# Kernel tuning notes

Hardware: AMD Instinct MI355X
Metric: run time of the kernel (lower is better)

The kernel has to match this reference:

```python
import jax, jax.numpy as jnp
import numpy as np
import math

NB_STEPS = 50  # matches init kwarg nb_steps


def cc_quadrature(nb_steps):
    # Clenshaw-Curtis weights/nodes, identical to UMNN's compute_cc_weights.
    lam = np.arange(nb_steps + 1, dtype=np.float64).reshape(-1, 1)
    lam = np.cos((lam @ lam.T) * math.pi / nb_steps)
    lam[:, 0] = 0.5
    lam[:, -1] = 0.5 * lam[:, -1]
    lam = lam * 2.0 / nb_steps
    W = np.arange(nb_steps + 1, dtype=np.float64).reshape(-1, 1)
    W[np.arange(1, nb_steps + 1, 2)] = 0
    W = 2.0 / (1.0 - W ** 2)
    W[0] = 1
    W[np.arange(1, nb_steps + 1, 2)] = 0
    cc_weights = (lam.T @ W).astype(np.float32)                 # [K, 1]
    steps = np.cos(np.arange(nb_steps + 1, dtype=np.float64).reshape(-1, 1)
                   * math.pi / nb_steps).astype(np.float32)     # [K, 1]
    return jnp.asarray(cc_weights), jnp.asarray(steps)


def integrand_mlp(xh, W1, b1, W2, b2, W3, b3, W4, b4):
    y = jax.nn.relu(jnp.einsum('bkd,hd->bkh', xh, W1) + b1)
    y = jax.nn.relu(jnp.einsum('bkh,gh->bkg', y, W2) + b2)
    y = jax.nn.relu(jnp.einsum('bkg,fg->bkf', y, W3) + b3)
    y = jnp.einsum('bkf,of->bko', y, W4) + b4
    return jax.nn.elu(y) + 1.0


def setup_inputs() -> dict:
    key = jax.random.key(0)
    ks = jax.random.split(key, 10)
    B, HD, IN_D = 16384, 128, 64
    x = jax.random.normal(ks[0], (B, 1), dtype=jnp.float32)
    h = jax.random.normal(ks[1], (B, IN_D - 1), dtype=jnp.float32)
    def lin(k, fan_out, fan_in):
        return jax.random.normal(k, (fan_out, fan_in), dtype=jnp.float32) / np.sqrt(fan_in)
    return {
        'x': x, 'h': h,
        'W1': lin(ks[2], HD, IN_D), 'b1': jax.random.normal(ks[3], (HD,), dtype=jnp.float32) * 0.01,
        'W2': lin(ks[4], HD, HD),   'b2': jax.random.normal(ks[5], (HD,), dtype=jnp.float32) * 0.01,
        'W3': lin(ks[6], HD, HD),   'b3': jax.random.normal(ks[7], (HD,), dtype=jnp.float32) * 0.01,
        'W4': lin(ks[8], 1, HD),    'b4': jax.random.normal(ks[9], (1,), dtype=jnp.float32) * 0.01,
    }


def reference(x, h, W1, b1, W2, b2, W3, b3, W4, b4):
    cc_w, steps = cc_quadrature(NB_STEPS)          # [K,1], [K,1]
    xmax = jnp.max(x) + 10.0
    x0 = x                                          # [B,1]
    xT = jnp.zeros_like(x) + xmax                   # xfinal broadcast
    # quadrature points X_steps: [B, K, 1]
    X = x0[:, None, :] + (xT - x0)[:, None, :] * (steps[None, :, :] + 1.0) * 0.5
    B, K = X.shape[0], X.shape[1]
    hK = jnp.broadcast_to(h[:, None, :], (B, K, h.shape[1]))
    xh = jnp.concatenate([X, hK], axis=-1)          # [B, K, in_d]
    f = integrand_mlp(xh, W1, b1, W2, b2, W3, b3, W4, b4)  # [B, K, 1]
    z = jnp.sum(f * cc_w[None, :, :], axis=1)       # [B, 1]
    return z * (xT - x0) * 0.5
```

## Files before the change

### kernel.cpp

```cpp
#include <hip/hip_runtime.h>
#include <hip/hip_bf16.h>
#include <math.h>


#define B_N    16384
#define KQ     51
#define HD     128
#define IND    64
#define BLK    128
#define RPB    16
#define GRID   (B_N / RPB)
#define TPB    (RPB * KQ / 16)

typedef __attribute__((ext_vector_type(8))) short short8;
typedef __attribute__((ext_vector_type(4))) float f32x4;

union S8U { short8 s8; unsigned u[4]; };

__device__ __forceinline__ unsigned short f2bf(float f) {
    __hip_bfloat16 t = __float2bfloat16(f);
    return *reinterpret_cast<unsigned short*>(&t);
}

#if defined(__gfx950__) && defined(__has_builtin)
#if __has_builtin(__builtin_amdgcn_cvt_pk_bf16_f32)
#define HAVE_PK_BF16 1
#endif
#endif

__device__ __forceinline__ unsigned pk_bf16(float lo, float hi) {
#ifdef HAVE_PK_BF16
    typedef __attribute__((ext_vector_type(2))) __bf16 bfv2;
    bfv2 r = __builtin_amdgcn_cvt_pk_bf16_f32(lo, hi);
    return *reinterpret_cast<unsigned*>(&r);
#else
    return (unsigned)f2bf(lo) | ((unsigned)f2bf(hi) << 16);
#endif
}

__device__ __forceinline__ float bf_lo(unsigned u) {
    return __uint_as_float(u << 16);
}
__device__ __forceinline__ float bf_hi(unsigned u) {
    return __uint_as_float(u & 0xffff0000u);
}

__launch_bounds__(BLK, 2)
__global__ void umnn_fused(const float* __restrict__ x,  const float* __restrict__ h,
                           const float* __restrict__ W1, const float* __restrict__ b1,
                           const float* __restrict__ W2, const float* __restrict__ b2,
                           const float* __restrict__ W3, const float* __restrict__ b3,
                           const float* __restrict__ W4, const float* __restrict__ b4,
                           float* __restrict__ out)
{
    __shared__ __align__(16) float hpL[RPB * HD];
    __shared__ __align__(16) char  y2x[2][4096];
    __shared__ __align__(16) float hshT[63 * 20];
    __shared__ float vs[RPB * KQ + 16];
    __shared__ float xL[RPB];
    __shared__ float sSteps[KQ], sCcw[KQ];
    __shared__ float red2[2];

    const int tid  = threadIdx.x;
    const int w    = tid >> 6;
    const int lane = tid & 63;
    const int q    = lane >> 4;
    const int lm   = lane & 15;
    const int swz  = lm & 7;
    const int rowBase = blockIdx.x * RPB;

    if (tid < KQ) {
        const int j = tid;
        const float pi50 = 0.06283185307179586f;
        sSteps[j] = __cosf((float)j * pi50);
        float s = 0.0f;
        for (int i = 0; i <= 50; i += 2) {
            float Wi = (i == 0) ? 1.0f : 2.0f / (1.0f - (float)(i * i));
            float lam;
            if (j == 0) lam = 0.5f;
            else {
                int mp = (i * j) % 100;
                lam = __cosf((float)mp * pi50);
                if (j == 50) lam *= 0.5f;
            }
            s += (lam * 0.04f) * Wi;
        }
        sCcw[j] = s;
    }
    {
        const f32x4* x4 = (const f32x4*)x;
        float mx = -1e30f;
        for (int i = tid; i < B_N / 4; i += BLK) {
            f32x4 v = x4[i];
            mx = fmaxf(fmaxf(mx, fmaxf(v[0], v[1])), fmaxf(v[2], v[3]));
        }
        #pragma unroll
        for (int d = 32; d > 0; d >>= 1) mx = fmaxf(mx, __shfl_xor(mx, d));
        if (lane == 0) red2[w] = mx;
    }
    for (int i = tid; i < RPB * 63; i += BLK) {
        int r = i / 63, d = i - r * 63;
        hshT[d * 20 + r] = h[rowBase * 63 + i];
    }
    if (tid < RPB) xL[tid] = x[rowBase + tid];
    __syncthreads();

    const float xmax = fmaxf(red2[0], red2[1]) + 10.0f;

    {
        const int n = tid;
        float acc[RPB];
        const float b1v = b1[n];
        #pragma unroll
        for (int r = 0; r < RPB; ++r) acc[r] = b1v;
        const float* wr = W1 + n * IND + 1;
        #pragma unroll 1
        for (int d = 0; d < IND - 1; ++d) {
            float wv = wr[d];
            const float* ht = hshT + d * 20;
            #pragma unroll
            for (int rc = 0; rc < RPB / 4; ++rc) {
                f32x4 hv = *(const f32x4*)(ht + rc * 4);
                acc[rc * 4 + 0] = fmaf(wv, hv[0], acc[rc * 4 + 0]);
                acc[rc * 4 + 1] = fmaf(wv, hv[1], acc[rc * 4 + 1]);
                acc[rc * 4 + 2] = fmaf(wv, hv[2], acc[rc * 4 + 2]);
                acc[rc * 4 + 3] = fmaf(wv, hv[3], acc[rc * 4 + 3]);
            }
        }
        #pragma unroll
        for (int r = 0; r < RPB; ++r) hpL[r * HD + n] = acc[r];
    }
    __syncthreads();

    if (w == 0) {
        float w1x[32];
        #pragma unroll
        for (int kk = 0; kk < 4; ++kk)
            #pragma unroll
            for (int j = 0; j < 8; ++j)
                w1x[kk * 8 + j] = W1[(kk * 32 + q * 8 + j) * IND];

        short8  W2A[8][4];
        unsigned b2p[16];
        #pragma unroll
        for (int nt = 0; nt < 8; ++nt) {
            #pragma unroll
            for (int kk = 0; kk < 4; ++kk) {
                const float* p2 = W2 + (nt * 16 + lm) * HD + kk * 32 + q * 8;
                S8U a2;
                #pragma unroll
                for (int j = 0; j < 4; ++j)
                    a2.u[j] = pk_bf16(p2[2 * j], p2[2 * j + 1]);
                W2A[nt][kk] = a2.s8;
            }
            b2p[2 * nt + 0] = pk_bf16(b2[nt * 16 + q * 4 + 0], b2[nt * 16 + q * 4 + 1]);
            b2p[2 * nt + 1] = pk_bf16(b2[nt * 16 + q * 4 + 2], b2[nt * 16 + q * 4 + 3]);
        }

        #pragma unroll 1
        for (int tt = 0; tt < TPB; ++tt) {
            const int s    = tt * 16 + lm;
            const unsigned row = (unsigned)s / KQ;
            const int k    = s - (int)row * KQ;
            const float x0 = xL[row];
            const float X  = fmaf((xmax - x0) * 0.5f, sSteps[k] + 1.0f, x0);
            short8 Y1[4];
            #pragma unroll
            for (int kk = 0; kk < 4; ++kk) {
                const float* hp = hpL + row * HD + kk * 32 + q * 8;
                f32x4 ha = *(const f32x4*)hp;
                f32x4 hb = *(const f32x4*)(hp + 4);
                S8U u;
                u.u[0] = pk_bf16(fmaxf(fmaf(X, w1x[kk*8+0], ha[0]), 0.f),
                                 fmaxf(fmaf(X, w1x[kk*8+1], ha[1]), 0.f));
                u.u[1] = pk_bf16(fmaxf(fmaf(X, w1x[kk*8+2], ha[2]), 0.f),
                                 fmaxf(fmaf(X, w1x[kk*8+3], ha[3]), 0.f));
                u.u[2] = pk_bf16(fmaxf(fmaf(X, w1x[kk*8+4], hb[0]), 0.f),
                                 fmaxf(fmaf(X, w1x[kk*8+5], hb[1]), 0.f));
                u.u[3] = pk_bf16(fmaxf(fmaf(X, w1x[kk*8+6], hb[2]), 0.f),
                                 fmaxf(fmaf(X, w1x[kk*8+7], hb[3]), 0.f));
                Y1[kk] = u.s8;
            }

            f32x4 C[8];
            #pragma unroll
            for (int nt = 0; nt < 8; ++nt) {
                unsigned u0 = b2p[2 * nt], u1 = b2p[2 * nt + 1];
                C[nt][0] = bf_lo(u0); C[nt][1] = bf_hi(u0);
                C[nt][2] = bf_lo(u1); C[nt][3] = bf_hi(u1);
            }
            #pragma unroll
            for (int kk = 0; kk < 4; ++kk)
                #pragma unroll
                for (int nt = 0; nt < 8; ++nt)
                    C[nt] = __builtin_amdgcn_mfma_f32_16x16x32_bf16(W2A[nt][kk], Y1[kk], C[nt], 0, 0, 0);

            char* myY2 = y2x[tt & 1];
            #pragma unroll
            for (int nt = 0; nt < 8; ++nt) {
                unsigned lo = pk_bf16(fmaxf(C[nt][0], 0.f), fmaxf(C[nt][1], 0.f));
                unsigned hi = pk_bf16(fmaxf(C[nt][2], 0.f), fmaxf(C[nt][3], 0.f));
                *(int2*)(myY2 + lm * 256 + (((2*nt + (q>>1)) ^ swz) << 4) + ((q & 1) << 3))
                    = make_int2((int)lo, (int)hi);
            }
            __syncthreads();
        }
    } else {
        short8  W3A[8][4];
        unsigned b3p[16];
        f32x4   W4c[8];
        #pragma unroll
        for (int nt = 0; nt < 8; ++nt) {
            #pragma unroll
            for (int kk = 0; kk < 4; ++kk) {
                const float* p3 = W3 + (nt * 16 + lm) * HD + kk * 32 + q * 8;
                S8U a3;
                #pragma unroll
                for (int j = 0; j < 4; ++j)
                    a3.u[j] = pk_bf16(p3[2 * j], p3[2 * j + 1]);
                W3A[nt][kk] = a3.s8;
            }
            b3p[2 * nt + 0] = pk_bf16(b3[nt * 16 + q * 4 + 0], b3[nt * 16 + q * 4 + 1]);
            b3p[2 * nt + 1] = pk_bf16(b3[nt * 16 + q * 4 + 2], b3[nt * 16 + q * 4 + 3]);
            W4c[nt] = *(const f32x4*)(W4 + nt * 16 + q * 4);
        }
        const float b4v = b4[0];

        #pragma unroll 1
        for (int tt = 0; tt < TPB; ++tt) {
            __syncthreads();
            const char* myY2 = y2x[tt & 1];
            short8 Y2[4];
            #pragma unroll
            for (int kk = 0; kk < 4; ++kk)
                Y2[kk] = *(const short8*)(myY2 + lm * 256 + (((kk*4 + q) ^ swz) << 4));

            f32x4 C[8];
            #pragma unroll
            for (int nt = 0; nt < 8; ++nt) {
                unsigned u0 = b3p[2 * nt], u1 = b3p[2 * nt + 1];
                C[nt][0] = bf_lo(u0); C[nt][1] = bf_hi(u0);
                C[nt][2] = bf_lo(u1); C[nt][3] = bf_hi(u1);
            }
            #pragma unroll
            for (int kk = 0; kk < 4; ++kk)
                #pragma unroll
                for (int nt = 0; nt < 8; ++nt)
                    C[nt] = __builtin_amdgcn_mfma_f32_16x16x32_bf16(W3A[nt][kk], Y2[kk], C[nt], 0, 0, 0);

            float p = 0.f;
            #pragma unroll
            for (int nt = 0; nt < 8; ++nt) {
                p = fmaf(fmaxf(C[nt][0], 0.f), W4c[nt][0], p);
                p = fmaf(fmaxf(C[nt][1], 0.f), W4c[nt][1], p);
                p = fmaf(fmaxf(C[nt][2], 0.f), W4c[nt][2], p);
                p = fmaf(fmaxf(C[nt][3], 0.f), W4c[nt][3], p);
            }
            p += __shfl_xor(p, 16);
            p += __shfl_xor(p, 32);
            if (lane < 16) vs[tt * 16 + lm] = p;
        }

        {
            const int r   = lane >> 2;
            const int sub = lane & 3;
            float a = 0.f;
            #pragma unroll 1
            for (int j = 0; j < 13; ++j) {
                int k = sub + 4 * j;
                if (k < KQ) {
                    float y4 = vs[r * KQ + k] + b4v;
                    float f  = (y4 > 0.f) ? (y4 + 1.f) : __expf(y4);
                    a = fmaf(f, sCcw[k], a);
                }
            }
            a += __shfl_xor(a, 1);
            a += __shfl_xor(a, 2);
            if (sub == 0)
                out[rowBase + r] = a * (xmax - xL[r]) * 0.5f;
        }
    }
}

extern "C" void kernel_launch(void* const* d_in, const int* in_sizes, int n_in,
                              void* d_out, int out_size, void* d_ws, size_t ws_size,
                              hipStream_t stream)
{
    const float* x  = (const float*)d_in[0];
    const float* h  = (const float*)d_in[1];
    const float* W1 = (const float*)d_in[2];
    const float* b1 = (const float*)d_in[3];
    const float* W2 = (const float*)d_in[4];
    const float* b2 = (const float*)d_in[5];
    const float* W3 = (const float*)d_in[6];
    const float* b3 = (const float*)d_in[7];
    const float* W4 = (const float*)d_in[8];
    const float* b4 = (const float*)d_in[9];
    float* out = (float*)d_out;

    umnn_fused<<<GRID, BLK, 0, stream>>>(x, h, W1, b1, W2, b2, W3, b3,
                                         W4, b4, out);
}
```

Before: 172.7 us.

## Split layer-2/3 MFMA work across four waves with a triple-buffered Y1 pipeline

Doubles the block to four waves. Two waves compute layer 2 and two compute layer 3, each wave owning half of the output tiles. Layer-1 activations are now built cooperatively into a three-slot shared-memory ring one tile ahead, and the layer-3 partial dot products land in two buffers that are summed in the final quadrature step. This is meant to remove the serial producer/consumer imbalance and the halved MFMA throughput per wave, at the cost of more barriers, more shared memory, and fewer registers per thread under launch_bounds(256,3).

```diff
diff --git a/kernel.cpp b/kernel.cpp
--- a/kernel.cpp
+++ b/kernel.cpp
@@ -7,10 +7,10 @@
 #define KQ     51
 #define HD     128
 #define IND    64
-#define BLK    128
+#define BLK    256
 #define RPB    16
 #define GRID   (B_N / RPB)
-#define TPB    (RPB * KQ / 16)
+#define TPB    ((RPB * KQ) / 16)
 
 typedef __attribute__((ext_vector_type(8))) short short8;
 typedef __attribute__((ext_vector_type(4))) float f32x4;
@@ -45,7 +45,7 @@
     return __uint_as_float(u & 0xffff0000u);
 }
 
-__launch_bounds__(BLK, 2)
+__launch_bounds__(BLK, 3)
 __global__ void umnn_fused(const float* __restrict__ x,  const float* __restrict__ h,
                            const float* __restrict__ W1, const float* __restrict__ b1,
                            const float* __restrict__ W2, const float* __restrict__ b2,
@@ -54,12 +54,13 @@
                            float* __restrict__ out)
 {
     __shared__ __align__(16) float hpL[RPB * HD];
+    __shared__ __align__(16) char  y1x[3][4096];
     __shared__ __align__(16) char  y2x[2][4096];
     __shared__ __align__(16) float hshT[63 * 20];
-    __shared__ float vs[RPB * KQ + 16];
+    __shared__ float vs2[2][RPB * KQ + 16];
     __shared__ float xL[RPB];
     __shared__ float sSteps[KQ], sCcw[KQ];
-    __shared__ float red2[2];
+    __shared__ float red4[4];
 
     const int tid  = threadIdx.x;
     const int w    = tid >> 6;
@@ -67,6 +68,8 @@
     const int q    = lane >> 4;
     const int lm   = lane & 15;
     const int swz  = lm & 7;
+    const bool isL2 = (w < 2);
+    const int ntB  = (w & 1) * 4;
     const int rowBase = blockIdx.x * RPB;
 
     if (tid < KQ) {
@@ -87,6 +90,39 @@
         }
         sCcw[j] = s;
     }
+
+    const float* Wsel = isL2 ? W2 : W3;
+    const float* bsel = isL2 ? b2 : b3;
+    short8  WA[4][4];
+    unsigned bp[8];
+    #pragma unroll
+    for (int nt = 0; nt < 4; ++nt) {
+        #pragma unroll
+        for (int kk = 0; kk < 4; ++kk) {
+            const float* p = Wsel + ((ntB + nt) * 16 + lm) * HD + kk * 32 + q * 8;
+            S8U a;
+            #pragma unroll
+            for (int j = 0; j < 4; ++j)
+                a.u[j] = pk_bf16(p[2 * j], p[2 * j + 1]);
+            WA[nt][kk] = a.s8;
+        }
+        bp[2 * nt + 0] = pk_bf16(bsel[(ntB + nt) * 16 + q * 4 + 0],
+                                 bsel[(ntB + nt) * 16 + q * 4 + 1]);
+        bp[2 * nt + 1] = pk_bf16(bsel[(ntB + nt) * 16 + q * 4 + 2],
+                                 bsel[(ntB + nt) * 16 + q * 4 + 3]);
+    }
+    f32x4 W4c[4];
+    if (!isL2) {
+        #pragma unroll
+        for (int nt = 0; nt < 4; ++nt)
+            W4c[nt] = *(const f32x4*)(W4 + (ntB + nt) * 16 + q * 4);
+    }
+    const float b4v = b4[0];
+    float w1x[8];
+    #pragma unroll
+    for (int j = 0; j < 8; ++j)
+        w1x[j] = W1[(w * 32 + q * 8 + j) * IND];
+
     {
         const f32x4* x4 = (const f32x4*)x;
         float mx = -1e30f;
@@ -96,7 +132,7 @@
         }
         #pragma unroll
         for (int d = 32; d > 0; d >>= 1) mx = fmaxf(mx, __shfl_xor(mx, d));
-        if (lane == 0) red2[w] = mx;
+        if (lane == 0) red4[w] = mx;
     }
     for (int i = tid; i < RPB * 63; i += BLK) {
         int r = i / 63, d = i - r * 63;
@@ -105,180 +141,145 @@
     if (tid < RPB) xL[tid] = x[rowBase + tid];
     __syncthreads();
 
-    const float xmax = fmaxf(red2[0], red2[1]) + 10.0f;
+    const float xmax = fmaxf(fmaxf(red4[0], red4[1]),
+                             fmaxf(red4[2], red4[3])) + 10.0f;
 
     {
-        const int n = tid;
-        float acc[RPB];
+        const int n  = tid & 127;
+        const int rh = (tid >> 7) * 8;
+        float acc[8];
         const float b1v = b1[n];
         #pragma unroll
-        for (int r = 0; r < RPB; ++r) acc[r] = b1v;
+        for (int r = 0; r < 8; ++r) acc[r] = b1v;
         const float* wr = W1 + n * IND + 1;
         #pragma unroll 1
         for (int d = 0; d < IND - 1; ++d) {
             float wv = wr[d];
-            const float* ht = hshT + d * 20;
+            const float* ht = hshT + d * 20 + rh;
+            f32x4 hv0 = *(const f32x4*)ht;
+            f32x4 hv1 = *(const f32x4*)(ht + 4);
+            acc[0] = fmaf(wv, hv0[0], acc[0]);
+            acc[1] = fmaf(wv, hv0[1], acc[1]);
+            acc[2] = fmaf(wv, hv0[2], acc[2]);
+            acc[3] = fmaf(wv, hv0[3], acc[3]);
+            acc[4] = fmaf(wv, hv1[0], acc[4]);
+            acc[5] = fmaf(wv, hv1[1], acc[5]);
+            acc[6] = fmaf(wv, hv1[2], acc[6]);
+            acc[7] = fmaf(wv, hv1[3], acc[7]);
+        }
+        #pragma unroll
+        for (int r = 0; r < 8; ++r) hpL[(rh + r) * HD + n] = acc[r];
+    }
+    __syncthreads();
+
+    int rdOff[4];
+    #pragma unroll
+    for (int kk = 0; kk < 4; ++kk)
+        rdOff[kk] = lm * 256 + (((kk * 4 + q) ^ swz) << 4);
+    const int bldOff = lm * 256 + (((w * 4 + q) ^ swz) << 4);
+    int wrOff[4];
+    #pragma unroll
+    for (int nt = 0; nt < 4; ++nt)
+        wrOff[nt] = lm * 256 + (((2 * (ntB + nt) + (q >> 1)) ^ swz) << 4) + ((q & 1) << 3);
+    float* vsW = vs2[w & 1];
+
+    auto buildY1 = [&](int ib, char* dst) {
+        const int s   = ib * 16 + lm;
+        const int row = s / KQ;
+        const int k   = s - row * KQ;
+        const float x0 = xL[row];
+        const float X  = fmaf((xmax - x0) * 0.5f, sSteps[k] + 1.0f, x0);
+        const float* hp = hpL + row * HD + w * 32 + q * 8;
+        f32x4 ha = *(const f32x4*)hp;
+        f32x4 hb = *(const f32x4*)(hp + 4);
+        S8U u;
+        u.u[0] = pk_bf16(fmaxf(fmaf(X, w1x[0], ha[0]), 0.f),
+                         fmaxf(fmaf(X, w1x[1], ha[1]), 0.f));
+        u.u[1] = pk_bf16(fmaxf(fmaf(X, w1x[2], ha[2]), 0.f),
+                         fmaxf(fmaf(X, w1x[3], ha[3]), 0.f));
+        u.u[2] = pk_bf16(fmaxf(fmaf(X, w1x[4], hb[0]), 0.f),
+                         fmaxf(fmaf(X, w1x[5], hb[1]), 0.f));
+        u.u[3] = pk_bf16(fmaxf(fmaf(X, w1x[6], hb[2]), 0.f),
+                         fmaxf(fmaf(X, w1x[7], hb[3]), 0.f));
+        *(short8*)(dst + bldOff) = u.s8;
+    };
+
+    buildY1(0, y1x[0]);
+    buildY1(1, y1x[1]);
+    __syncthreads();
+
+    int br = 0, bw = 2;
+    #pragma unroll 1
+    for (int i = 0; i <= TPB; ++i) {
+        const bool act = isL2 ? (i < TPB) : (i >= 1);
+        const char* src = isL2 ? (const char*)y1x[br]
+                               : (const char*)y2x[(i + 1) & 1];
+        short8 Yf[4];
+        if (act) {
             #pragma unroll
-            for (int rc = 0; rc < RPB / 4; ++rc) {
-                f32x4 hv = *(const f32x4*)(ht + rc * 4);
-                acc[rc * 4 + 0] = fmaf(wv, hv[0], acc[rc * 4 + 0]);
-                acc[rc * 4 + 1] = fmaf(wv, hv[1], acc[rc * 4 + 1]);
-                acc[rc * 4 + 2] = fmaf(wv, hv[2], acc[rc * 4 + 2]);
-                acc[rc * 4 + 3] = fmaf(wv, hv[3], acc[rc * 4 + 3]);
-            }
-        }
-        #pragma unroll
-        for (int r = 0; r < RPB; ++r) hpL[r * HD + n] = acc[r];
-    }
-    __syncthreads();
-
-    if (w == 0) {
-        float w1x[32];
-        #pragma unroll
-        for (int kk = 0; kk < 4; ++kk)
+            for (int kk = 0; kk < 4; ++kk)
+                Yf[kk] = *(const short8*)(src + rdOff[kk]);
+        }
+        if (i + 2 < TPB) buildY1(i + 2, y1x[bw]);
+
+        if (act) {
+            f32x4 C[4];
             #pragma unroll
-            for (int j = 0; j < 8; ++j)
-                w1x[kk * 8 + j] = W1[(kk * 32 + q * 8 + j) * IND];
-
-        short8  W2A[8][4];
-        unsigned b2p[16];
-        #pragma unroll
-        for (int nt = 0; nt < 8; ++nt) {
-            #pragma unroll
-            for (int kk = 0; kk < 4; ++kk) {
-                const float* p2 = W2 + (nt * 16 + lm) * HD + kk * 32 + q * 8;
-                S8U a2;
-                #pragma unroll
-                for (int j = 0; j < 4; ++j)
-                    a2.u[j] = pk_bf16(p2[2 * j], p2[2 * j + 1]);
-                W2A[nt][kk] = a2.s8;
-            }
-            b2p[2 * nt + 0] = pk_bf16(b2[nt * 16 + q * 4 + 0], b2[nt * 16 + q * 4 + 1]);
-            b2p[2 * nt + 1] = pk_bf16(b2[nt * 16 + q * 4 + 2], b2[nt * 16 + q * 4 + 3]);
-        }
-
-        #pragma unroll 1
-        for (int tt = 0; tt < TPB; ++tt) {
-            const int s    = tt * 16 + lm;
-            const unsigned row = (unsigned)s / KQ;
-            const int k    = s - (int)row * KQ;
-            const float x0 = xL[row];
-            const float X  = fmaf((xmax - x0) * 0.5f, sSteps[k] + 1.0f, x0);
-            short8 Y1[4];
-            #pragma unroll
-            for (int kk = 0; kk < 4; ++kk) {
-                const float* hp = hpL + row * HD + kk * 32 + q * 8;
-                f32x4 ha = *(const f32x4*)hp;
-                f32x4 hb = *(const f32x4*)(hp + 4);
-                S8U u;
-                u.u[0] = pk_bf16(fmaxf(fmaf(X, w1x[kk*8+0], ha[0]), 0.f),
-                                 fmaxf(fmaf(X, w1x[kk*8+1], ha[1]), 0.f));
-                u.u[1] = pk_bf16(fmaxf(fmaf(X, w1x[kk*8+2], ha[2]), 0.f),
-                                 fmaxf(fmaf(X, w1x[kk*8+3], ha[3]), 0.f));
-                u.u[2] = pk_bf16(fmaxf(fmaf(X, w1x[kk*8+4], hb[0]), 0.f),
-                                 fmaxf(fmaf(X, w1x[kk*8+5], hb[1]), 0.f));
-                u.u[3] = pk_bf16(fmaxf(fmaf(X, w1x[kk*8+6], hb[2]), 0.f),
-                                 fmaxf(fmaf(X, w1x[kk*8+7], hb[3]), 0.f));
-                Y1[kk] = u.s8;
-            }
-
-            f32x4 C[8];
-            #pragma unroll
-            for (int nt = 0; nt < 8; ++nt) {
-                unsigned u0 = b2p[2 * nt], u1 = b2p[2 * nt + 1];
+            for (int nt = 0; nt < 4; ++nt) {
+                unsigned u0 = bp[2 * nt], u1 = bp[2 * nt + 1];
                 C[nt][0] = bf_lo(u0); C[nt][1] = bf_hi(u0);
                 C[nt][2] = bf_lo(u1); C[nt][3] = bf_hi(u1);
             }
             #pragma unroll
             for (int kk = 0; kk < 4; ++kk)
                 #pragma unroll
-                for (int nt = 0; nt < 8; ++nt)
-                    C[nt] = __builtin_amdgcn_mfma_f32_16x16x32_bf16(W2A[nt][kk], Y1[kk], C[nt], 0, 0, 0);
-
-            char* myY2 = y2x[tt & 1];
-            #pragma unroll
-            for (int nt = 0; nt < 8; ++nt) {
-                unsigned lo = pk_bf16(fmaxf(C[nt][0], 0.f), fmaxf(C[nt][1], 0.f));
-                unsigned hi = pk_bf16(fmaxf(C[nt][2], 0.f), fmaxf(C[nt][3], 0.f));
-                *(int2*)(myY2 + lm * 256 + (((2*nt + (q>>1)) ^ swz) << 4) + ((q & 1) << 3))
-                    = make_int2((int)lo, (int)hi);
+                for (int nt = 0; nt < 4; ++nt)
+                    C[nt] = __builtin_amdgcn_mfma_f32_16x16x32_bf16(WA[nt][kk], Yf[kk], C[nt], 0, 0, 0);
+
+            if (isL2) {
+                char* d2 = y2x[i & 1];
+                #pragma unroll
+                for (int nt = 0; nt < 4; ++nt) {
+                    unsigned lo = pk_bf16(fmaxf(C[nt][0], 0.f), fmaxf(C[nt][1], 0.f));
+                    unsigned hi = pk_bf16(fmaxf(C[nt][2], 0.f), fmaxf(C[nt][3], 0.f));
+                    *(int2*)(d2 + wrOff[nt]) = make_int2((int)lo, (int)hi);
+                }
+            } else {
+                float pa = 0.f;
+                #pragma unroll
+                for (int nt = 0; nt < 4; ++nt) {
+                    pa = fmaf(fmaxf(C[nt][0], 0.f), W4c[nt][0], pa);
+                    pa = fmaf(fmaxf(C[nt][1], 0.f), W4c[nt][1], pa);
+                    pa = fmaf(fmaxf(C[nt][2], 0.f), W4c[nt][2], pa);
+                    pa = fmaf(fmaxf(C[nt][3], 0.f), W4c[nt][3], pa);
+                }
+                pa += __shfl_xor(pa, 16);
+                pa += __shfl_xor(pa, 32);
+                if (lane < 16) vsW[(i - 1) * 16 + lm] = pa;
             }
-            __syncthreads();
-        }
-    } else {
-        short8  W3A[8][4];
-        unsigned b3p[16];
-        f32x4   W4c[8];
-        #pragma unroll
-        for (int nt = 0; nt < 8; ++nt) {
-            #pragma unroll
-            for (int kk = 0; kk < 4; ++kk) {
-                const float* p3 = W3 + (nt * 16 + lm) * HD + kk * 32 + q * 8;
-                S8U a3;
-                #pragma unroll
-                for (int j = 0; j < 4; ++j)
-                    a3.u[j] = pk_bf16(p3[2 * j], p3[2 * j + 1]);
-                W3A[nt][kk] = a3.s8;
+        }
+        __syncthreads();
+        br = (br == 2) ? 0 : br + 1;
+        bw = (bw == 2) ? 0 : bw + 1;
+    }
+
+    if (w == 0) {
+        const int r   = lane >> 2;
+        const int sub = lane & 3;
+        float a = 0.f;
+        #pragma unroll 1
+        for (int j = 0; j < 13; ++j) {
+            int k = sub + 4 * j;
+            if (k < KQ) {
+                float y4 = vs2[0][r * KQ + k] + vs2[1][r * KQ + k] + b4v;
+                float f  = (y4 > 0.f) ? (y4 + 1.f) : __expf(y4);
+                a = fmaf(f, sCcw[k], a);
             }
-            b3p[2 * nt + 0] = pk_bf16(b3[nt * 16 + q * 4 + 0], b3[nt * 16 + q * 4 + 1]);
-            b3p[2 * nt + 1] = pk_bf16(b3[nt * 16 + q * 4 + 2], b3[nt * 16 + q * 4 + 3]);
-            W4c[nt] = *(const f32x4*)(W4 + nt * 16 + q * 4);
-        }
-        const float b4v = b4[0];
-
-        #pragma unroll 1
-        for (int tt = 0; tt < TPB; ++tt) {
-            __syncthreads();
-            const char* myY2 = y2x[tt & 1];
-            short8 Y2[4];
-            #pragma unroll
-            for (int kk = 0; kk < 4; ++kk)
-                Y2[kk] = *(const short8*)(myY2 + lm * 256 + (((kk*4 + q) ^ swz) << 4));
-
-            f32x4 C[8];
-            #pragma unroll
-            for (int nt = 0; nt < 8; ++nt) {
-                unsigned u0 = b3p[2 * nt], u1 = b3p[2 * nt + 1];
-                C[nt][0] = bf_lo(u0); C[nt][1] = bf_hi(u0);
-                C[nt][2] = bf_lo(u1); C[nt][3] = bf_hi(u1);
-            }
-            #pragma unroll
-            for (int kk = 0; kk < 4; ++kk)
-                #pragma unroll
-                for (int nt = 0; nt < 8; ++nt)
-                    C[nt] = __builtin_amdgcn_mfma_f32_16x16x32_bf16(W3A[nt][kk], Y2[kk], C[nt], 0, 0, 0);
-
-            float p = 0.f;
-            #pragma unroll
-            for (int nt = 0; nt < 8; ++nt) {
-                p = fmaf(fmaxf(C[nt][0], 0.f), W4c[nt][0], p);
-                p = fmaf(fmaxf(C[nt][1], 0.f), W4c[nt][1], p);
-                p = fmaf(fmaxf(C[nt][2], 0.f), W4c[nt][2], p);
-                p = fmaf(fmaxf(C[nt][3], 0.f), W4c[nt][3], p);
-            }
-            p += __shfl_xor(p, 16);
-            p += __shfl_xor(p, 32);
-            if (lane < 16) vs[tt * 16 + lm] = p;
-        }
-
-        {
-            const int r   = lane >> 2;
-            const int sub = lane & 3;
-            float a = 0.f;
-            #pragma unroll 1
-            for (int j = 0; j < 13; ++j) {
-                int k = sub + 4 * j;
-                if (k < KQ) {
-                    float y4 = vs[r * KQ + k] + b4v;
-                    float f  = (y4 > 0.f) ? (y4 + 1.f) : __expf(y4);
-                    a = fmaf(f, sCcw[k], a);
-                }
-            }
-            a += __shfl_xor(a, 1);
-            a += __shfl_xor(a, 2);
-            if (sub == 0)
-                out[rowBase + r] = a * (xmax - xL[r]) * 0.5f;
-        }
+        }
+        a += __shfl_xor(a, 1);
+        a += __shfl_xor(a, 2);
+        if (sub == 0)
+            out[rowBase + r] = a * (xmax - xL[r]) * 0.5f;
     }
 }
 
```

New measurement: 210.7 us. 1.22x slower.

## Process two tiles per barrier between layer-2 and layer-3 warps

Applied to the files above, without the earlier changes.

The producer/consumer warp pipeline now handles two 16-row tiles per synchronisation step, so the number of block barriers is roughly halved, and the shared Y2 buffer grows to 8 KB per stage. The producer builds the second tile's Y1 while the first tile's MFMAs run, and the consumer issues both tiles' LDS reads up front. MFMA sections are wrapped in s_setprio to favour matrix issue. Swizzled offsets are precomputed once. The cost is more shared memory and register pressure, which may hurt occupancy under launch bounds of 2 blocks per CU.

```diff
diff --git a/kernel.cpp b/kernel.cpp
--- a/kernel.cpp
+++ b/kernel.cpp
@@ -10,7 +10,8 @@
 #define BLK    128
 #define RPB    16
 #define GRID   (B_N / RPB)
-#define TPB    (RPB * KQ / 16)
+#define TPB    ((RPB * KQ) / 16)
+#define NPAIR  26
 
 typedef __attribute__((ext_vector_type(8))) short short8;
 typedef __attribute__((ext_vector_type(4))) float f32x4;
@@ -54,7 +55,7 @@
                            float* __restrict__ out)
 {
     __shared__ __align__(16) float hpL[RPB * HD];
-    __shared__ __align__(16) char  y2x[2][4096];
+    __shared__ __align__(16) char  y2x[2][8192];
     __shared__ __align__(16) float hshT[63 * 20];
     __shared__ float vs[RPB * KQ + 16];
     __shared__ float xL[RPB];
@@ -156,15 +157,17 @@
             b2p[2 * nt + 0] = pk_bf16(b2[nt * 16 + q * 4 + 0], b2[nt * 16 + q * 4 + 1]);
             b2p[2 * nt + 1] = pk_bf16(b2[nt * 16 + q * 4 + 2], b2[nt * 16 + q * 4 + 3]);
         }
-
-        #pragma unroll 1
-        for (int tt = 0; tt < TPB; ++tt) {
-            const int s    = tt * 16 + lm;
+        int wrOff[8];
+        #pragma unroll
+        for (int nt = 0; nt < 8; ++nt)
+            wrOff[nt] = lm * 256 + (((2 * nt + (q >> 1)) ^ swz) << 4) + ((q & 1) << 3);
+
+        auto buildY1 = [&](int t, short8* Y) {
+            const int s   = t * 16 + lm;
             const unsigned row = (unsigned)s / KQ;
-            const int k    = s - (int)row * KQ;
+            const int k   = s - (int)row * KQ;
             const float x0 = xL[row];
             const float X  = fmaf((xmax - x0) * 0.5f, sSteps[k] + 1.0f, x0);
-            short8 Y1[4];
             #pragma unroll
             for (int kk = 0; kk < 4; ++kk) {
                 const float* hp = hpL + row * HD + kk * 32 + q * 8;
@@ -179,29 +182,66 @@
                                  fmaxf(fmaf(X, w1x[kk*8+5], hb[1]), 0.f));
                 u.u[3] = pk_bf16(fmaxf(fmaf(X, w1x[kk*8+6], hb[2]), 0.f),
                                  fmaxf(fmaf(X, w1x[kk*8+7], hb[3]), 0.f));
-                Y1[kk] = u.s8;
-            }
-
-            f32x4 C[8];
-            #pragma unroll
-            for (int nt = 0; nt < 8; ++nt) {
-                unsigned u0 = b2p[2 * nt], u1 = b2p[2 * nt + 1];
-                C[nt][0] = bf_lo(u0); C[nt][1] = bf_hi(u0);
-                C[nt][2] = bf_lo(u1); C[nt][3] = bf_hi(u1);
-            }
-            #pragma unroll
-            for (int kk = 0; kk < 4; ++kk)
-                #pragma unroll
-                for (int nt = 0; nt < 8; ++nt)
-                    C[nt] = __builtin_amdgcn_mfma_f32_16x16x32_bf16(W2A[nt][kk], Y1[kk], C[nt], 0, 0, 0);
-
-            char* myY2 = y2x[tt & 1];
-            #pragma unroll
-            for (int nt = 0; nt < 8; ++nt) {
-                unsigned lo = pk_bf16(fmaxf(C[nt][0], 0.f), fmaxf(C[nt][1], 0.f));
-                unsigned hi = pk_bf16(fmaxf(C[nt][2], 0.f), fmaxf(C[nt][3], 0.f));
-                *(int2*)(myY2 + lm * 256 + (((2*nt + (q>>1)) ^ swz) << 4) + ((q & 1) << 3))
-                    = make_int2((int)lo, (int)hi);
+                Y[kk] = u.s8;
+            }
+        };
+
+        #pragma unroll 1
+        for (int j = 0; j <= NPAIR; ++j) {
+            if (j < NPAIR) {
+                const int t0 = 2 * j;
+                const bool two = (t0 + 1 < TPB);
+                char* d2 = y2x[j & 1];
+
+                short8 Y1a[4];
+                buildY1(t0, Y1a);
+
+                f32x4 C[8];
+                #pragma unroll
+                for (int nt = 0; nt < 8; ++nt) {
+                    unsigned u0 = b2p[2 * nt], u1 = b2p[2 * nt + 1];
+                    C[nt][0] = bf_lo(u0); C[nt][1] = bf_hi(u0);
+                    C[nt][2] = bf_lo(u1); C[nt][3] = bf_hi(u1);
+                }
+                __builtin_amdgcn_s_setprio(1);
+                #pragma unroll
+                for (int kk = 0; kk < 4; ++kk)
+                    #pragma unroll
+                    for (int nt = 0; nt < 8; ++nt)
+                        C[nt] = __builtin_amdgcn_mfma_f32_16x16x32_bf16(W2A[nt][kk], Y1a[kk], C[nt], 0, 0, 0);
+                __builtin_amdgcn_s_setprio(0);
+
+                short8 Y1b[4];
+                if (two) buildY1(t0 + 1, Y1b);
+
+                #pragma unroll
+                for (int nt = 0; nt < 8; ++nt) {
+                    unsigned lo = pk_bf16(fmaxf(C[nt][0], 0.f), fmaxf(C[nt][1], 0.f));
+                    unsigned hi = pk_bf16(fmaxf(C[nt][2], 0.f), fmaxf(C[nt][3], 0.f));
+                    *(int2*)(d2 + wrOff[nt]) = make_int2((int)lo, (int)hi);
+                }
+
+                if (two) {
+                    #pragma unroll
+                    for (int nt = 0; nt < 8; ++nt) {
+                        unsigned u0 = b2p[2 * nt], u1 = b2p[2 * nt + 1];
+                        C[nt][0] = bf_lo(u0); C[nt][1] = bf_hi(u0);
+                        C[nt][2] = bf_lo(u1); C[nt][3] = bf_hi(u1);
+                    }
+                    __builtin_amdgcn_s_setprio(1);
+                    #pragma unroll
+                    for (int kk = 0; kk < 4; ++kk)
+                        #pragma unroll
+                        for (int nt = 0; nt < 8; ++nt)
+                            C[nt] = __builtin_amdgcn_mfma_f32_16x16x32_bf16(W2A[nt][kk], Y1b[kk], C[nt], 0, 0, 0);
+                    __builtin_amdgcn_s_setprio(0);
+                    #pragma unroll
+                    for (int nt = 0; nt < 8; ++nt) {
+                        unsigned lo = pk_bf16(fmaxf(C[nt][0], 0.f), fmaxf(C[nt][1], 0.f));
+                        unsigned hi = pk_bf16(fmaxf(C[nt][2], 0.f), fmaxf(C[nt][3], 0.f));
+                        *(int2*)(d2 + 4096 + wrOff[nt]) = make_int2((int)lo, (int)hi);
+                    }
+                }
             }
             __syncthreads();
         }
@@ -225,40 +265,85 @@
             W4c[nt] = *(const f32x4*)(W4 + nt * 16 + q * 4);
         }
         const float b4v = b4[0];
+        int rdOff[4];
+        #pragma unroll
+        for (int kk = 0; kk < 4; ++kk)
+            rdOff[kk] = lm * 256 + (((kk * 4 + q) ^ swz) << 4);
 
         #pragma unroll 1
-        for (int tt = 0; tt < TPB; ++tt) {
+        for (int j = 0; j <= NPAIR; ++j) {
+            if (j >= 1) {
+                const int pr = j - 1;
+                const int t0 = 2 * pr;
+                const bool two = (t0 + 1 < TPB);
+                const char* s2 = y2x[pr & 1];
+
+                short8 Ya[4], Yb[4];
+                #pragma unroll
+                for (int kk = 0; kk < 4; ++kk)
+                    Ya[kk] = *(const short8*)(s2 + rdOff[kk]);
+                if (two) {
+                    #pragma unroll
+                    for (int kk = 0; kk < 4; ++kk)
+                        Yb[kk] = *(const short8*)(s2 + 4096 + rdOff[kk]);
+                }
+
+                f32x4 C[8];
+                #pragma unroll
+                for (int nt = 0; nt < 8; ++nt) {
+                    unsigned u0 = b3p[2 * nt], u1 = b3p[2 * nt + 1];
+                    C[nt][0] = bf_lo(u0); C[nt][1] = bf_hi(u0);
+                    C[nt][2] = bf_lo(u1); C[nt][3] = bf_hi(u1);
+                }
+                __builtin_amdgcn_s_setprio(1);
+                #pragma unroll
+                for (int kk = 0; kk < 4; ++kk)
+                    #pragma unroll
+                    for (int nt = 0; nt < 8; ++nt)
+                        C[nt] = __builtin_amdgcn_mfma_f32_16x16x32_bf16(W3A[nt][kk], Ya[kk], C[nt], 0, 0, 0);
+                __builtin_amdgcn_s_setprio(0);
+
+                float pa = 0.f;
+                #pragma unroll
+                for (int nt = 0; nt < 8; ++nt) {
+                    pa = fmaf(fmaxf(C[nt][0], 0.f), W4c[nt][0], pa);
+                    pa = fmaf(fmaxf(C[nt][1], 0.f), W4c[nt][1], pa);
+                    pa = fmaf(fmaxf(C[nt][2], 0.f), W4c[nt][2], pa);
+                    pa = fmaf(fmaxf(C[nt][3], 0.f), W4c[nt][3], pa);
+                }
+                pa += __shfl_xor(pa, 16);
+                pa += __shfl_xor(pa, 32);
+                if (lane < 16) vs[t0 * 16 + lm] = pa;
+
+                if (two) {
+                    #pragma unroll
+                    for (int nt = 0; nt < 8; ++nt) {
+                        unsigned u0 = b3p[2 * nt], u1 = b3p[2 * nt + 1];
+                        C[nt][0] = bf_lo(u0); C[nt][1] = bf_hi(u0);
+                        C[nt][2] = bf_lo(u1); C[nt][3] = bf_hi(u1);
+                    }
+                    __builtin_amdgcn_s_setprio(1);
+                    #pragma unroll
+                    for (int kk = 0; kk < 4; ++kk)
+                        #pragma unroll
+                        for (int nt = 0; nt < 8; ++nt)
+                            C[nt] = __builtin_amdgcn_mfma_f32_16x16x32_bf16(W3A[nt][kk], Yb[kk], C[nt], 0, 0, 0);
+                    __builtin_amdgcn_s_setprio(0);
+
+                    float pb = 0.f;
+                    #pragma unroll
+                    for (int nt = 0; nt < 8; ++nt) {
+                        pb = fmaf(fmaxf(C[nt][0], 0.f), W4c[nt][0], pb);
+                        pb = fmaf(fmaxf(C[nt][1], 0.f), W4c[nt][1], pb);
+                        pb = fmaf(fmaxf(C[nt][2], 0.f), W4c[nt][2], pb);
+                        pb = fmaf(fmaxf(C[nt][3], 0.f), W4c[nt][3], pb);
+                    }
+                    pb += __shfl_xor(pb, 16);
+                    pb += __shfl_xor(pb, 32);
+                    if (lane < 16) vs[(t0 + 1) * 16 + lm] = pb;
+                }
+            }
             __syncthreads();
-            const char* myY2 = y2x[tt & 1];
-            short8 Y2[4];
-            #pragma unroll
-            for (int kk = 0; kk < 4; ++kk)
-                Y2[kk] = *(const short8*)(myY2 + lm * 256 + (((kk*4 + q) ^ swz) << 4));
-
-            f32x4 C[8];
-            #pragma unroll
-            for (int nt = 0; nt < 8; ++nt) {
-                unsigned u0 = b3p[2 * nt], u1 = b3p[2 * nt + 1];
-                C[nt][0] = bf_lo(u0); C[nt][1] = bf_hi(u0);
-                C[nt][2] = bf_lo(u1); C[nt][3] = bf_hi(u1);
-            }
-            #pragma unroll
-            for (int kk = 0; kk < 4; ++kk)
-                #pragma unroll
-                for (int nt = 0; nt < 8; ++nt)
-                    C[nt] = __builtin_amdgcn_mfma_f32_16x16x32_bf16(W3A[nt][kk], Y2[kk], C[nt], 0, 0, 0);
-
-            float p = 0.f;
-            #pragma unroll
-            for (int nt = 0; nt < 8; ++nt) {
-                p = fmaf(fmaxf(C[nt][0], 0.f), W4c[nt][0], p);
-                p = fmaf(fmaxf(C[nt][1], 0.f), W4c[nt][1], p);
-                p = fmaf(fmaxf(C[nt][2], 0.f), W4c[nt][2], p);
-                p = fmaf(fmaxf(C[nt][3], 0.f), W4c[nt][3], p);
-            }
-            p += __shfl_xor(p, 16);
-            p += __shfl_xor(p, 32);
-            if (lane < 16) vs[tt * 16 + lm] = p;
         }
 
         {
```

New measurement: 200.6 us. 1.16x slower.
